# Optimization experiments

Hardware: AMD Instinct MI355X
Metric: run time of the kernel (lower is better)

Reference implementation:

```python
import jax, jax.numpy as jnp
import numpy as np

B, T_ENC, T_DEC = 64, 100, 50
L = 512      # lstm_size
E = 512      # input_encoding_size
H = 512      # att_hidden_size
R = 8        # num_review_steps
V_TOK = 30001  # token_cnt + 1 embedding rows
V_OUT = 30000  # word_cnt


def _lstm_maxout(s, c):
    # ARNet/neuraltalk2 LSTMCore: 5*L preactivations, maxout input transform
    i = jax.nn.sigmoid(s[:, :L])
    f = jax.nn.sigmoid(s[:, L:2 * L])
    o = jax.nn.sigmoid(s[:, 2 * L:3 * L])
    t = jnp.maximum(s[:, 3 * L:4 * L], s[:, 4 * L:])
    c2 = f * c + i * t
    return o * jnp.tanh(c2), c2


def _attend(feats, h, Wa2a, ba2a, Wh2a, bh2a, Watt, batt):
    # feats: [B, A, F], h: [B, L] -> context [B, F]
    p = jnp.tanh(feats @ Wa2a + ba2a + (h @ Wh2a + bh2a)[:, None, :])  # [B,A,H]
    e = jnp.squeeze(p @ Watt, -1) + batt                               # [B,A]
    a = jax.nn.softmax(e, axis=-1)
    return jnp.einsum('ba,baf->bf', a, feats)


def setup_inputs() -> dict:
    key = jax.random.key(0)
    ks = iter(jax.random.split(key, 48))
    g = lambda shape: jax.random.normal(next(ks), shape, jnp.float32) * 0.05
    z = lambda shape: jnp.zeros(shape, jnp.float32)
    return {
        'code_matrix': jax.random.randint(next(ks), (B, T_ENC), 0, V_TOK),
        'comment_matrix': jax.random.randint(next(ks), (B, T_DEC), 0, V_TOK),
        'current_comment_mask_cuda': jnp.ones((B, T_DEC), jnp.float32),
        'embed': jax.random.uniform(next(ks), (V_TOK, E), jnp.float32, -0.1, 0.1),
        'enc_Wi': g((E, 5 * L)), 'enc_bi': z((5 * L,)),
        'enc_Wh': g((L, 5 * L)), 'enc_bh': z((5 * L,)),
        'rev_Wh': g((R, L, 5 * L)), 'rev_bh': z((R, 5 * L)),
        'rev_Wa': g((R, L, 5 * L)), 'rev_ba': z((R, 5 * L)),
        'rev_Wa2a': g((R, L, H)), 'rev_ba2a': z((R, H)),
        'rev_Wh2a': g((R, L, H)), 'rev_bh2a': z((R, H)),
        'rev_Watt': g((R, H, 1)), 'rev_batt': z((R,)),
        'dec_Wi': g((E, 5 * L)), 'dec_bi': z((5 * L,)),
        'dec_Wh': g((L, 5 * L)), 'dec_bh': z((5 * L,)),
        'dec_Wa': g((L, 5 * L)), 'dec_ba': z((5 * L,)),
        'dec_Wa2a': g((L, H)), 'dec_ba2a': z((H,)),
        'dec_Wh2a': g((L, H)), 'dec_bh2a': z((H,)),
        'dec_Watt': g((H, 1)), 'dec_batt': z(()),
        'logit_W': jax.random.uniform(next(ks), (L, V_OUT), jnp.float32, -0.1, 0.1),
        'logit_b': z((V_OUT,)),
    }


def reference(code_matrix, comment_matrix, current_comment_mask_cuda, embed,
              enc_Wi, enc_bi, enc_Wh, enc_bh,
              rev_Wh, rev_bh, rev_Wa, rev_ba, rev_Wa2a, rev_ba2a,
              rev_Wh2a, rev_bh2a, rev_Watt, rev_batt,
              dec_Wi, dec_bi, dec_Wh, dec_bh, dec_Wa, dec_ba,
              dec_Wa2a, dec_ba2a, dec_Wh2a, dec_bh2a, dec_Watt, dec_batt,
              logit_W, logit_b):
    del current_comment_mask_cuda  # only used by scheduled sampling (ss_prob=0)
    Bsz = code_matrix.shape[0]
    h0 = jnp.zeros((Bsz, L), embed.dtype)
    c0 = jnp.zeros((Bsz, L), embed.dtype)

    # ---- encode ----
    enc_x = embed[code_matrix]  # [B, T_enc, E]

    def enc_step(carry, xt):
        h, c = carry
        s = xt @ enc_Wi + enc_bi + h @ enc_Wh + enc_bh
        h2, c2 = _lstm_maxout(s, c)
        return (h2, c2), h2

    (h_enc, c_enc), enc_hs = jax.lax.scan(enc_step, (h0, c0), jnp.swapaxes(enc_x, 0, 1))
    enc_hs = jnp.swapaxes(enc_hs, 0, 1)  # [B, T_enc, L]

    # ---- review (distinct params per step; scan over stacked params) ----
    def rev_step(carry, p):
        h, c = carry
        Wh, bh, Wa, ba, Wa2a, ba2a, Wh2a, bh2a, Watt, batt = p
        att_v = _attend(enc_hs, h, Wa2a, ba2a, Wh2a, bh2a, Watt, batt)
        s = h @ Wh + bh + att_v @ Wa + ba
        h2, c2 = _lstm_maxout(s, c)
        return (h2, c2), h2

    rev_params = (rev_Wh, rev_bh, rev_Wa, rev_ba, rev_Wa2a, rev_ba2a,
                  rev_Wh2a, rev_bh2a, rev_Watt, rev_batt)
    _, thought = jax.lax.scan(rev_step, (h_enc, c_enc), rev_params)
    thought = jnp.swapaxes(thought, 0, 1)  # [B, R, L]

    # ---- decode (teacher forcing; decode_state starts from encode_state) ----
    dec_x = embed[comment_matrix]  # [B, T_dec, E]

    def dec_step(carry, xt):
        h, c = carry
        att_v = _attend(thought, h, dec_Wa2a, dec_ba2a, dec_Wh2a, dec_bh2a, dec_Watt, dec_batt)
        s = xt @ dec_Wi + dec_bi + h @ dec_Wh + dec_bh + att_v @ dec_Wa + dec_ba
        h2, c2 = _lstm_maxout(s, c)
        logp = jax.nn.log_softmax(h2 @ logit_W + logit_b, axis=-1)
        return (h2, c2), logp

    _, logps = jax.lax.scan(dec_step, (h_enc, c_enc), jnp.swapaxes(dec_x, 0, 1))
    return jnp.swapaxes(logps, 0, 1)  # [B, T_dec, V_OUT]
```

## Files before the change

kernel.cpp:

```cpp
#include <hip/hip_runtime.h>
#include <math.h>
#include <stdint.h>

#define BB     64
#define TENC   100
#define TDEC   50
#define LDIM   512
#define EE     512
#define HDIM   512
#define FIVEL  2560
#define RSTEPS 8
#define VOUT   30000

typedef __attribute__((ext_vector_type(8))) short short8v;
typedef __attribute__((ext_vector_type(4))) float floatx4;

__device__ __forceinline__ float sigmoidf_(float x) { return 1.0f / (1.0f + __expf(-x)); }
__device__ __forceinline__ unsigned short f2bf(float x) {
    unsigned u = __float_as_uint(x);
    u += 0x7FFFu + ((u >> 16) & 1u);
    return (unsigned short)(u >> 16);
}
__device__ __forceinline__ float bf2f(unsigned short h) {
    return __uint_as_float(((unsigned)h) << 16);
}

__global__ __launch_bounds__(128)
void gather_embed(const float* __restrict__ embed, const int* __restrict__ tok,
                  int T, unsigned short* __restrict__ X)
{
    int m = blockIdx.x, t = m / BB, b = m % BB;
    const float* src = embed + (size_t)tok[b * T + t] * EE;
    float4 v = *(const float4*)(src + threadIdx.x * 4);
    ushort4 o = { f2bf(v.x), f2bf(v.y), f2bf(v.z), f2bf(v.w) };
    *(ushort4*)(X + (size_t)m * EE + threadIdx.x * 4) = o;
}

__global__ __launch_bounds__(256)
void conv_transpose(const float* __restrict__ W, unsigned short* __restrict__ WT,
                    int K, int N, int ldWT, int kofs)
{
    __shared__ float tile[32][33];
    int n0 = blockIdx.x * 32, k0 = blockIdx.y * 32;
    int tx = threadIdx.x & 31, ty = threadIdx.x >> 5;
    #pragma unroll
    for (int i = 0; i < 4; ++i) {
        int k = k0 + ty + i * 8, n = n0 + tx;
        tile[ty + i * 8][tx] = (n < N) ? W[(size_t)k * N + n] : 0.f;
    }
    __syncthreads();
    #pragma unroll
    for (int i = 0; i < 4; ++i) {
        int n = n0 + ty + i * 8, k = k0 + tx;
        if (n < N) WT[(size_t)n * ldWT + kofs + k] = f2bf(tile[tx][ty + i * 8]);
    }
}

__global__ __launch_bounds__(256)
void gemm_bf16(const unsigned short* __restrict__ A, const unsigned short* __restrict__ BT,
               const float* __restrict__ bias, float* __restrict__ C,
               unsigned short* __restrict__ Cb, int N, int K, long ldc, int remap)
{
    __shared__ unsigned short lds[2][128][32];
    const int tid  = threadIdx.x;
    const int wave = tid >> 6, lane = tid & 63;
    const int m0 = blockIdx.y * 128, n0 = blockIdx.x * 128;
    const int wr = wave >> 1, wc = wave & 1;

    floatx4 acc[4][4] = {};

    const int sr  = lane >> 2;
    const int scp = lane & 3;

    for (int k0 = 0; k0 < K; k0 += 32) {
        #pragma unroll
        for (int half = 0; half < 2; ++half) {
            int rbase = wave * 32 + half * 16;
            int r = rbase + sr;
            int c = scp ^ ((r >> 1) & 3);
            const unsigned short* ga = A + (size_t)(m0 + r) * K + k0 + c * 8;
            int nr = n0 + r; if (nr >= N) nr = 0;
            const unsigned short* gb = BT + (size_t)nr * K + k0 + c * 8;
            __builtin_amdgcn_global_load_lds(
                (const __attribute__((address_space(1))) void*)ga,
                (__attribute__((address_space(3))) void*)&lds[0][rbase][0], 16, 0, 0);
            __builtin_amdgcn_global_load_lds(
                (const __attribute__((address_space(1))) void*)gb,
                (__attribute__((address_space(3))) void*)&lds[1][rbase][0], 16, 0, 0);
        }
        __syncthreads();

        short8v af[4], bv[4];
        #pragma unroll
        for (int i = 0; i < 4; ++i) {
            int ra = wr * 64 + i * 16 + (lane & 15);
            int ca = (lane >> 4) ^ ((ra >> 1) & 3);
            af[i] = *(const short8v*)&lds[0][ra][ca * 8];
            int rb = wc * 64 + i * 16 + (lane & 15);
            int cb = (lane >> 4) ^ ((rb >> 1) & 3);
            bv[i] = *(const short8v*)&lds[1][rb][cb * 8];
        }
        #pragma unroll
        for (int i = 0; i < 4; ++i)
            #pragma unroll
            for (int j = 0; j < 4; ++j)
                acc[i][j] = __builtin_amdgcn_mfma_f32_16x16x32_bf16(af[i], bv[j], acc[i][j], 0, 0, 0);
        __syncthreads();
    }

    const int crow0 = m0 + wr * 64 + (lane >> 4) * 4;
    const int ccol0 = n0 + wc * 64 + (lane & 15);
    #pragma unroll
    for (int i = 0; i < 4; ++i) {
        #pragma unroll
        for (int j = 0; j < 4; ++j) {
            int col = ccol0 + j * 16;
            if (col < N) {
                float bval = bias ? bias[col] : 0.f;
                #pragma unroll
                for (int rr = 0; rr < 4; ++rr) {
                    int m = crow0 + i * 16 + rr;
                    long orow = m;
                    if (remap) { int t = m >> 6, b = m & 63; orow = (long)b * TDEC + t; }
                    float v = acc[i][j][rr] + bval;
                    if (Cb) Cb[orow * ldc + col] = f2bf(v);
                    else    C [orow * ldc + col] = v;
                }
            }
        }
    }
}

template<int NF, int MODE>
__global__ __launch_bounds__(256)
void smallgemm(const unsigned short* __restrict__ a0,
               const unsigned short* __restrict__ a1,
               const unsigned short* __restrict__ a2,
               const unsigned short* __restrict__ BT, int ldBT,
               const unsigned short* __restrict__ pre,
               const float* __restrict__ b0, const float* __restrict__ b1,
               const float* __restrict__ b2,
               const float* __restrict__ c_in, float* __restrict__ c_out,
               unsigned short* __restrict__ h_out, unsigned short* __restrict__ h_copy,
               float* __restrict__ f_out)
{
    __shared__ unsigned short Alds[64][128];
    __shared__ unsigned short Blds[NF * 16][128];
    const int tid = threadIdx.x;
    const int wave = tid >> 6, lane = tid & 63;
    const int c0 = blockIdx.x * 16;

    const unsigned short* segs[3] = {a0, a1, a2};
    const int nseg = a2 ? 3 : (a1 ? 2 : 1);
    const int NO = nseg * 4;

    floatx4 acc[NF];
    #pragma unroll
    for (int g = 0; g < NF; ++g) acc[g] = (floatx4){0.f, 0.f, 0.f, 0.f};

    short8v ra[4], rb[NF];

    #define LOAD_TILE(ot_) do {                                                \
        int seg_ = (ot_) >> 2, k0_ = ((ot_) & 3) * 128;                        \
        const unsigned short* A_ = segs[seg_];                                 \
        _Pragma("unroll")                                                      \
        for (int j = 0; j < 4; ++j) {                                          \
            int idx = tid + j * 256; int r = idx >> 4, ch = idx & 15;          \
            ra[j] = *(const short8v*)(A_ + (size_t)r * 512 + k0_ + ch * 8);    \
        }                                                                      \
        _Pragma("unroll")                                                      \
        for (int j = 0; j < NF; ++j) {                                         \
            int idx = tid + j * 256; int r = idx >> 4, ch = idx & 15;          \
            int grow = (r >> 4) * 512 + c0 + (r & 15);                         \
            rb[j] = *(const short8v*)(BT + (size_t)grow * ldBT + seg_ * 512 + k0_ + ch * 8); \
        }                                                                      \
    } while (0)

    LOAD_TILE(0);
    for (int ot = 0; ot < NO; ++ot) {
        __syncthreads();
        #pragma unroll
        for (int j = 0; j < 4; ++j) {
            int idx = tid + j * 256; int r = idx >> 4, ch = idx & 15;
            *(short8v*)&Alds[r][(ch ^ (r & 7)) * 8] = ra[j];
        }
        #pragma unroll
        for (int j = 0; j < NF; ++j) {
            int idx = tid + j * 256; int r = idx >> 4, ch = idx & 15;
            *(short8v*)&Blds[r][(ch ^ (r & 7)) * 8] = rb[j];
        }
        __syncthreads();
        if (ot + 1 < NO) LOAD_TILE(ot + 1);

        const int arow = wave * 16 + (lane & 15);
        const int q = lane >> 4;
        #pragma unroll
        for (int kk = 0; kk < 4; ++kk) {
            int ch = kk * 4 + q;
            short8v af = *(const short8v*)&Alds[arow][(ch ^ (arow & 7)) * 8];
            #pragma unroll
            for (int g = 0; g < NF; ++g) {
                int brow = g * 16 + (lane & 15);
                short8v bf = *(const short8v*)&Blds[brow][(ch ^ (brow & 7)) * 8];
                acc[g] = __builtin_amdgcn_mfma_f32_16x16x32_bf16(af, bf, acc[g], 0, 0, 0);
            }
        }
    }
    #undef LOAD_TILE

    const int m = wave * 16 + (lane >> 4) * 4;
    const int c = c0 + (lane & 15);
    if (MODE == 1) {
        float bv = b0 ? b0[c] : 0.f;
        #pragma unroll
        for (int rr = 0; rr < 4; ++rr)
            f_out[(size_t)(m + rr) * 512 + c] = acc[0][rr] + bv;
    } else {
        float bias[5];
        #pragma unroll
        for (int g = 0; g < 5; ++g) {
            float v = b0[g * 512 + c];
            if (b1) v += b1[g * 512 + c];
            if (b2) v += b2[g * 512 + c];
            bias[g] = v;
        }
        #pragma unroll
        for (int rr = 0; rr < 4; ++rr) {
            int row = m + rr;
            float s[5];
            #pragma unroll
            for (int g = 0; g < 5; ++g) {
                s[g] = acc[g][rr] + bias[g];
                if (pre) s[g] += bf2f(pre[(size_t)row * FIVEL + g * 512 + c]);
            }
            float ig = sigmoidf_(s[0]), fg = sigmoidf_(s[1]), og = sigmoidf_(s[2]);
            float tt = fmaxf(s[3], s[4]);
            float c2 = fg * c_in[(size_t)row * 512 + c] + ig * tt;
            float h2 = og * tanhf(c2);
            c_out[(size_t)row * 512 + c] = c2;
            unsigned short hb = f2bf(h2);
            h_out[(size_t)row * 512 + c] = hb;
            if (h_copy) h_copy[(size_t)row * 512 + c] = hb;
        }
    }
}

__global__ __launch_bounds__(256)
void attend(const unsigned short* __restrict__ proj, const float* __restrict__ hproj,
            const unsigned short* __restrict__ feats, const float* __restrict__ Watt,
            unsigned short* __restrict__ att_v, int A)
{
    __shared__ float hp[512];
    __shared__ float wa[512];
    __shared__ float ealpha[128];
    const int b = blockIdx.x;
    const int tid = threadIdx.x;
    for (int i = tid; i < 512; i += 256) { hp[i] = hproj[b * HDIM + i]; wa[i] = Watt[i]; }
    __syncthreads();
    const int wave = tid >> 6, lane = tid & 63;
    for (int a = wave; a < A; a += 4) {
        short8v pv = *(const short8v*)(proj + ((size_t)a * BB + b) * HDIM + lane * 8);
        float e = 0.f;
        #pragma unroll
        for (int j = 0; j < 8; ++j) {
            int hcol = lane * 8 + j;
            e += tanhf(bf2f((unsigned short)pv[j]) + hp[hcol]) * wa[hcol];
        }
        #pragma unroll
        for (int off = 32; off; off >>= 1) e += __shfl_xor(e, off);
        if (lane == 0) ealpha[a] = e;
    }
    __syncthreads();
    if (wave == 0) {
        float v1 = (lane < A) ? ealpha[lane] : -3.0e38f;
        float v2 = (lane + 64 < A) ? ealpha[lane + 64] : -3.0e38f;
        float m = fmaxf(v1, v2);
        #pragma unroll
        for (int off = 32; off; off >>= 1) m = fmaxf(m, __shfl_xor(m, off));
        float x1 = (lane < A) ? __expf(v1 - m) : 0.f;
        float x2 = (lane + 64 < A) ? __expf(v2 - m) : 0.f;
        float ssum = x1 + x2;
        #pragma unroll
        for (int off = 32; off; off >>= 1) ssum += __shfl_xor(ssum, off);
        float inv = 1.0f / ssum;
        if (lane < A) ealpha[lane] = x1 * inv;
        if (lane + 64 < A) ealpha[lane + 64] = x2 * inv;
    }
    __syncthreads();
    #pragma unroll
    for (int jj = 0; jj < 2; ++jj) {
        int l = tid + jj * 256;
        float acc = 0.f;
        for (int a = 0; a < A; ++a)
            acc += ealpha[a] * bf2f(feats[((size_t)a * BB + b) * LDIM + l]);
        att_v[(size_t)b * LDIM + l] = f2bf(acc);
    }
}

__global__ __launch_bounds__(256)
void log_softmax_(float* __restrict__ out)
{
    float* row = out + (size_t)blockIdx.x * VOUT;
    const int tid = threadIdx.x;
    float m = -3.0e38f, s = 0.f;
    for (int i = tid; i < VOUT / 4; i += 256) {
        float4 x = ((const float4*)row)[i];
        float xs[4] = {x.x, x.y, x.z, x.w};
        #pragma unroll
        for (int q = 0; q < 4; ++q) {
            float v = xs[q];
            if (v > m) { s = s * __expf(m - v) + 1.0f; m = v; }
            else       { s += __expf(v - m); }
        }
    }
    #pragma unroll
    for (int off = 32; off; off >>= 1) {
        float mo = __shfl_xor(m, off);
        float so = __shfl_xor(s, off);
        float mn = fmaxf(m, mo);
        s = s * __expf(m - mn) + so * __expf(mo - mn);
        m = mn;
    }
    __shared__ float ms[4], ss[4];
    const int wave = tid >> 6, lane = tid & 63;
    if (lane == 0) { ms[wave] = m; ss[wave] = s; }
    __syncthreads();
    float M2 = fmaxf(fmaxf(ms[0], ms[1]), fmaxf(ms[2], ms[3]));
    float S2 = ss[0] * __expf(ms[0] - M2) + ss[1] * __expf(ms[1] - M2) +
               ss[2] * __expf(ms[2] - M2) + ss[3] * __expf(ms[3] - M2);
    float lse = M2 + __logf(S2);
    for (int i = tid; i < VOUT / 4; i += 256) {
        float4 x = ((const float4*)row)[i];
        x.x -= lse; x.y -= lse; x.z -= lse; x.w -= lse;
        ((float4*)row)[i] = x;
    }
}

extern "C" void kernel_launch(void* const* d_in, const int* in_sizes, int n_in,
                              void* d_out_, int out_size, void* d_ws, size_t ws_size,
                              hipStream_t stream)
{
    const int*   code     = (const int*)  d_in[0];
    const int*   comment  = (const int*)  d_in[1];
    const float* embed    = (const float*)d_in[3];
    const float* enc_Wi   = (const float*)d_in[4];
    const float* enc_bi   = (const float*)d_in[5];
    const float* enc_Wh   = (const float*)d_in[6];
    const float* enc_bh   = (const float*)d_in[7];
    const float* rev_Wh   = (const float*)d_in[8];
    const float* rev_bh   = (const float*)d_in[9];
    const float* rev_Wa   = (const float*)d_in[10];
    const float* rev_ba   = (const float*)d_in[11];
    const float* rev_Wa2a = (const float*)d_in[12];
    const float* rev_ba2a = (const float*)d_in[13];
    const float* rev_Wh2a = (const float*)d_in[14];
    const float* rev_bh2a = (const float*)d_in[15];
    const float* rev_Watt = (const float*)d_in[16];
    const float* dec_Wi   = (const float*)d_in[18];
    const float* dec_bi   = (const float*)d_in[19];
    const float* dec_Wh   = (const float*)d_in[20];
    const float* dec_bh   = (const float*)d_in[21];
    const float* dec_Wa   = (const float*)d_in[22];
    const float* dec_ba   = (const float*)d_in[23];
    const float* dec_Wa2a = (const float*)d_in[24];
    const float* dec_ba2a = (const float*)d_in[25];
    const float* dec_Wh2a = (const float*)d_in[26];
    const float* dec_bh2a = (const float*)d_in[27];
    const float* dec_Watt = (const float*)d_in[28];
    const float* logit_W  = (const float*)d_in[30];
    const float* logit_b  = (const float*)d_in[31];
    float* out = (float*)d_out_;

    float* ws = (float*)d_ws;
    size_t off = 0;

    float* X = ws; off += 8192000;
    unsigned short* enc_pre_b = (unsigned short*)X;
    unsigned short* logit_WT  = (unsigned short*)X;

    float* U = ws + off; off += 2293760;
    unsigned short* WiT_enc    = (unsigned short*)U;
    unsigned short* enc_x_b    = (unsigned short*)(U + 655360);
    unsigned short* rev_proj_b = (unsigned short*)U;
    unsigned short* dec_h_b    = (unsigned short*)U;

    unsigned short* enc_hs_b = (unsigned short*)(ws + off); off += 1638400;
    unsigned short* encWhT   = (unsigned short*)(ws + off); off += 655360;
    unsigned short* revWcomb = (unsigned short*)(ws + off); off += 10485760;
    unsigned short* decWcomb = (unsigned short*)(ws + off); off += 1966080;
    unsigned short* revWT    = (unsigned short*)(ws + off); off += 1048576;
    unsigned short* decWT    = (unsigned short*)(ws + off); off += 131072;
    unsigned short* revWh2aT = (unsigned short*)(ws + off); off += 1048576;
    unsigned short* decWh2aT = (unsigned short*)(ws + off); off += 131072;
    unsigned short* dec_x_b  = (unsigned short*)(ws + off); off += 819200;
    unsigned short* thought_b= (unsigned short*)(ws + off); off += 131072;
    unsigned short* tproj_b  = (unsigned short*)(ws + off); off += 131072;
    unsigned short* h0_b     = (unsigned short*)(ws + off); off += 16384;
    unsigned short* hb0      = (unsigned short*)(ws + off); off += 16384;
    unsigned short* hb1      = (unsigned short*)(ws + off); off += 16384;
    unsigned short* attv_b   = (unsigned short*)(ws + off); off += 16384;
    float* cbuf[4];
    for (int i = 0; i < 4; ++i) { cbuf[i] = ws + off; off += 32768; }
    float* hproj = ws + off; off += 32768;
    if (ws_size < off * sizeof(float)) return;

    unsigned short* hb[2] = {hb0, hb1};
    const dim3 blk(256);

    hipMemsetAsync(cbuf[0], 0, (size_t)BB * LDIM * sizeof(float), stream);
    hipMemsetAsync(h0_b, 0, (size_t)BB * LDIM * sizeof(unsigned short), stream);

    gather_embed<<<TENC * BB, 128, 0, stream>>>(embed, code, TENC, enc_x_b);
    gather_embed<<<TDEC * BB, 128, 0, stream>>>(embed, comment, TDEC, dec_x_b);
    conv_transpose<<<dim3(80, 16), blk, 0, stream>>>(enc_Wi, WiT_enc, 512, FIVEL, 512, 0);
    conv_transpose<<<dim3(80, 16), blk, 0, stream>>>(enc_Wh, encWhT, 512, FIVEL, 512, 0);
    for (int r = 0; r < RSTEPS; ++r) {
        conv_transpose<<<dim3(80, 16), blk, 0, stream>>>(
            rev_Wh + (size_t)r * 1310720, revWcomb + (size_t)r * 2621440, 512, FIVEL, 1024, 0);
        conv_transpose<<<dim3(80, 16), blk, 0, stream>>>(
            rev_Wa + (size_t)r * 1310720, revWcomb + (size_t)r * 2621440, 512, FIVEL, 1024, 512);
        conv_transpose<<<dim3(16, 16), blk, 0, stream>>>(
            rev_Wa2a + (size_t)r * 262144, revWT + (size_t)r * 262144, 512, 512, 512, 0);
        conv_transpose<<<dim3(16, 16), blk, 0, stream>>>(
            rev_Wh2a + (size_t)r * 262144, revWh2aT + (size_t)r * 262144, 512, 512, 512, 0);
    }
    conv_transpose<<<dim3(80, 16), blk, 0, stream>>>(dec_Wi, decWcomb, 512, FIVEL, 1536, 0);
    conv_transpose<<<dim3(80, 16), blk, 0, stream>>>(dec_Wh, decWcomb, 512, FIVEL, 1536, 512);
    conv_transpose<<<dim3(80, 16), blk, 0, stream>>>(dec_Wa, decWcomb, 512, FIVEL, 1536, 1024);
    conv_transpose<<<dim3(16, 16), blk, 0, stream>>>(dec_Wa2a, decWT, 512, 512, 512, 0);
    conv_transpose<<<dim3(16, 16), blk, 0, stream>>>(dec_Wh2a, decWh2aT, 512, 512, 512, 0);

    gemm_bf16<<<dim3(FIVEL / 128, TENC * BB / 128), blk, 0, stream>>>(
        enc_x_b, WiT_enc, enc_bi, nullptr, enc_pre_b, FIVEL, EE, FIVEL, 0);

    for (int t = 0; t < TENC; ++t) {
        const unsigned short* hin = (t == 0) ? h0_b : enc_hs_b + (size_t)(t - 1) * 32768;
        smallgemm<5, 0><<<32, blk, 0, stream>>>(
            hin, nullptr, nullptr, encWhT, 512,
            enc_pre_b + (size_t)t * BB * FIVEL,
            enc_bh, nullptr, nullptr,
            cbuf[t & 1], cbuf[(t + 1) & 1],
            enc_hs_b + (size_t)t * 32768, nullptr, nullptr);
    }
    const unsigned short* h_enc = enc_hs_b + (size_t)(TENC - 1) * 32768;

    conv_transpose<<<dim3((VOUT + 31) / 32, 16), blk, 0, stream>>>(
        logit_W, logit_WT, 512, VOUT, 512, 0);

    const unsigned short* rh = h_enc;
    for (int r = 0; r < RSTEPS; ++r) {
        gemm_bf16<<<dim3(4, 50), blk, 0, stream>>>(
            enc_hs_b, revWT + (size_t)r * 262144, rev_ba2a + (size_t)r * HDIM,
            nullptr, rev_proj_b, HDIM, LDIM, HDIM, 0);
        smallgemm<1, 1><<<32, blk, 0, stream>>>(
            rh, nullptr, nullptr, revWh2aT + (size_t)r * 262144, 512,
            nullptr, rev_bh2a + (size_t)r * HDIM, nullptr, nullptr,
            nullptr, nullptr, nullptr, nullptr, hproj);
        attend<<<BB, blk, 0, stream>>>(rev_proj_b, hproj, enc_hs_b,
                                       rev_Watt + (size_t)r * HDIM, attv_b, TENC);
        const float* ci = (r == 0) ? cbuf[0] : cbuf[2 + ((r - 1) & 1)];
        smallgemm<5, 0><<<32, blk, 0, stream>>>(
            rh, attv_b, nullptr, revWcomb + (size_t)r * 2621440, 1024,
            nullptr, rev_bh + (size_t)r * FIVEL, rev_ba + (size_t)r * FIVEL, nullptr,
            ci, cbuf[2 + (r & 1)],
            hb[r & 1], thought_b + (size_t)r * 32768, nullptr);
        rh = hb[r & 1];
    }

    gemm_bf16<<<dim3(4, 4), blk, 0, stream>>>(
        thought_b, decWT, dec_ba2a, nullptr, tproj_b, HDIM, LDIM, HDIM, 0);

    const unsigned short* dh = h_enc;
    for (int t = 0; t < TDEC; ++t) {
        smallgemm<1, 1><<<32, blk, 0, stream>>>(
            dh, nullptr, nullptr, decWh2aT, 512,
            nullptr, dec_bh2a, nullptr, nullptr,
            nullptr, nullptr, nullptr, nullptr, hproj);
        attend<<<BB, blk, 0, stream>>>(tproj_b, hproj, thought_b, dec_Watt, attv_b, RSTEPS);
        const float* ci = (t == 0) ? cbuf[0] : cbuf[2 + ((t - 1) & 1)];
        smallgemm<5, 0><<<32, blk, 0, stream>>>(
            dec_x_b + (size_t)t * 32768, dh, attv_b, decWcomb, 1536,
            nullptr, dec_bi, dec_bh, dec_ba,
            ci, cbuf[2 + (t & 1)],
            hb[t & 1], dec_h_b + (size_t)t * 32768, nullptr);
        dh = hb[t & 1];
    }

    gemm_bf16<<<dim3((VOUT + 127) / 128, TDEC * BB / 128), blk, 0, stream>>>(
        dec_h_b, logit_WT, logit_b, out, nullptr, VOUT, LDIM, VOUT, 1);
    log_softmax_<<<TDEC * BB, blk, 0, stream>>>(out);
}
```

Before: 4.012 ms.

## Fuse recurrent LSTM loops into persistent kernels with grid barriers

Replaces the per-timestep launches of the encoder, review and decoder recurrences with three persistent kernels that sync between steps through a global atomic barrier. Cell state stays in registers, and attention plus the h2a projection are fused per pair of batch rows. The change also batches the review-step projection GEMM across all steps, merges the weight transposes into z-batched launches, and uses a fast exp-based tanh. The aim is to remove hundreds of kernel launch gaps; the cost is reliance on all blocks being co-resident for the spin barrier, and workspace buffers are now aliased.

```diff
diff --git a/kernel.cpp b/kernel.cpp
--- a/kernel.cpp
+++ b/kernel.cpp
@@ -14,8 +14,33 @@
 
 typedef __attribute__((ext_vector_type(8))) short short8v;
 typedef __attribute__((ext_vector_type(4))) float floatx4;
+typedef unsigned short ushort_t;
+
+static const size_t OFF_A        = 0;
+static const size_t OFF_WIT_ENC  = 8192000;
+static const size_t OFF_ENCX     = 8847360;
+static const size_t OFF_LOGWT    = 0;
+static const size_t OFF_DECH     = 7680000;
+static const size_t OFF_ENC_HS   = 13107200;
+static const size_t OFF_ENC_WHT  = 14745600;
+static const size_t OFF_REVWC    = 15400960;
+static const size_t OFF_DECWC    = 25886720;
+static const size_t OFF_REVWT    = 27852800;
+static const size_t OFF_DECWT    = 28901376;
+static const size_t OFF_REVWH2AT = 29032448;
+static const size_t OFF_DECWH2AT = 30081024;
+static const size_t OFF_DECX     = 30212096;
+static const size_t OFF_THOUGHT  = 31031296;
+static const size_t OFF_TPROJ    = 31162368;
+static const size_t OFF_HB0      = 31293440;
+static const size_t OFF_HB1      = 31309824;
+static const size_t OFF_ATTV     = 31326208;
+static const size_t OFF_CENC     = 31342592;
+static const size_t OFF_BAR      = 31375360;
+static const size_t WS_TOTAL     = 31375376;
 
 __device__ __forceinline__ float sigmoidf_(float x) { return 1.0f / (1.0f + __expf(-x)); }
+__device__ __forceinline__ float tanh_fast(float x) { return 1.0f - 2.0f / (__expf(2.0f * x) + 1.0f); }
 __device__ __forceinline__ unsigned short f2bf(float x) {
     unsigned u = __float_as_uint(x);
     u += 0x7FFFu + ((u >> 16) & 1u);
@@ -25,9 +50,28 @@
     return __uint_as_float(((unsigned)h) << 16);
 }
 
+__device__ __forceinline__ void gbar(unsigned int* bar, int nblk)
+{
+    __threadfence();
+    __syncthreads();
+    if (threadIdx.x == 0) {
+        unsigned int g = __hip_atomic_load(&bar[1], __ATOMIC_RELAXED, __HIP_MEMORY_SCOPE_AGENT);
+        unsigned int v = __hip_atomic_fetch_add(&bar[0], 1u, __ATOMIC_ACQ_REL, __HIP_MEMORY_SCOPE_AGENT);
+        if (v == (unsigned int)(nblk - 1)) {
+            __hip_atomic_store(&bar[0], 0u, __ATOMIC_RELAXED, __HIP_MEMORY_SCOPE_AGENT);
+            __hip_atomic_fetch_add(&bar[1], 1u, __ATOMIC_RELEASE, __HIP_MEMORY_SCOPE_AGENT);
+        } else {
+            while (__hip_atomic_load(&bar[1], __ATOMIC_RELAXED, __HIP_MEMORY_SCOPE_AGENT) == g)
+                __builtin_amdgcn_s_sleep(2);
+        }
+    }
+    __syncthreads();
+    __threadfence();
+}
+
 __global__ __launch_bounds__(128)
 void gather_embed(const float* __restrict__ embed, const int* __restrict__ tok,
-                  int T, unsigned short* __restrict__ X)
+                  int T, ushort_t* __restrict__ X)
 {
     int m = blockIdx.x, t = m / BB, b = m % BB;
     const float* src = embed + (size_t)tok[b * T + t] * EE;
@@ -37,9 +81,11 @@
 }
 
 __global__ __launch_bounds__(256)
-void conv_transpose(const float* __restrict__ W, unsigned short* __restrict__ WT,
-                    int K, int N, int ldWT, int kofs)
-{
+void conv_transpose(const float* __restrict__ W, ushort_t* __restrict__ WT,
+                    int N, int ldWT, int kofs, long Wz, long WTz)
+{
+    W  += (size_t)blockIdx.z * Wz;
+    WT += (size_t)blockIdx.z * WTz;
     __shared__ float tile[32][33];
     int n0 = blockIdx.x * 32, k0 = blockIdx.y * 32;
     int tx = threadIdx.x & 31, ty = threadIdx.x >> 5;
@@ -57,18 +103,17 @@
 }
 
 __global__ __launch_bounds__(256)
-void gemm_bf16(const unsigned short* __restrict__ A, const unsigned short* __restrict__ BT,
+void gemm_bf16(const ushort_t* __restrict__ A, const ushort_t* __restrict__ BT,
                const float* __restrict__ bias, float* __restrict__ C,
-               unsigned short* __restrict__ Cb, int N, int K, long ldc, int remap)
-{
-    __shared__ unsigned short lds[2][128][32];
+               ushort_t* __restrict__ Cb, int N, int K, long ldc, int remap)
+{
+    __shared__ ushort_t lds[2][128][32];
     const int tid  = threadIdx.x;
     const int wave = tid >> 6, lane = tid & 63;
     const int m0 = blockIdx.y * 128, n0 = blockIdx.x * 128;
     const int wr = wave >> 1, wc = wave & 1;
 
     floatx4 acc[4][4] = {};
-
     const int sr  = lane >> 2;
     const int scp = lane & 3;
 
@@ -78,9 +123,9 @@
             int rbase = wave * 32 + half * 16;
             int r = rbase + sr;
             int c = scp ^ ((r >> 1) & 3);
-            const unsigned short* ga = A + (size_t)(m0 + r) * K + k0 + c * 8;
+            const ushort_t* ga = A + (size_t)(m0 + r) * K + k0 + c * 8;
             int nr = n0 + r; if (nr >= N) nr = 0;
-            const unsigned short* gb = BT + (size_t)nr * K + k0 + c * 8;
+            const ushort_t* gb = BT + (size_t)nr * K + k0 + c * 8;
             __builtin_amdgcn_global_load_lds(
                 (const __attribute__((address_space(1))) void*)ga,
                 (__attribute__((address_space(3))) void*)&lds[0][rbase][0], 16, 0, 0);
@@ -131,67 +176,49 @@
     }
 }
 
-template<int NF, int MODE>
-__global__ __launch_bounds__(256)
-void smallgemm(const unsigned short* __restrict__ a0,
-               const unsigned short* __restrict__ a1,
-               const unsigned short* __restrict__ a2,
-               const unsigned short* __restrict__ BT, int ldBT,
-               const unsigned short* __restrict__ pre,
-               const float* __restrict__ b0, const float* __restrict__ b1,
-               const float* __restrict__ b2,
-               const float* __restrict__ c_in, float* __restrict__ c_out,
-               unsigned short* __restrict__ h_out, unsigned short* __restrict__ h_copy,
-               float* __restrict__ f_out)
-{
-    __shared__ unsigned short Alds[64][128];
-    __shared__ unsigned short Blds[NF * 16][128];
+__device__ __forceinline__ void lstm_accum(
+    const ushort_t* __restrict__ Aseg,
+    const ushort_t* __restrict__ BT,
+    const int ldBT, const int segk, const int c0, floatx4* acc,
+    ushort_t (*Alds)[128], ushort_t (*Blds)[128])
+{
     const int tid = threadIdx.x;
     const int wave = tid >> 6, lane = tid & 63;
-    const int c0 = blockIdx.x * 16;
-
-    const unsigned short* segs[3] = {a0, a1, a2};
-    const int nseg = a2 ? 3 : (a1 ? 2 : 1);
-    const int NO = nseg * 4;
-
-    floatx4 acc[NF];
-    #pragma unroll
-    for (int g = 0; g < NF; ++g) acc[g] = (floatx4){0.f, 0.f, 0.f, 0.f};
-
-    short8v ra[4], rb[NF];
-
-    #define LOAD_TILE(ot_) do {                                                \
-        int seg_ = (ot_) >> 2, k0_ = ((ot_) & 3) * 128;                        \
-        const unsigned short* A_ = segs[seg_];                                 \
-        _Pragma("unroll")                                                      \
-        for (int j = 0; j < 4; ++j) {                                          \
-            int idx = tid + j * 256; int r = idx >> 4, ch = idx & 15;          \
-            ra[j] = *(const short8v*)(A_ + (size_t)r * 512 + k0_ + ch * 8);    \
-        }                                                                      \
-        _Pragma("unroll")                                                      \
-        for (int j = 0; j < NF; ++j) {                                         \
-            int idx = tid + j * 256; int r = idx >> 4, ch = idx & 15;          \
-            int grow = (r >> 4) * 512 + c0 + (r & 15);                         \
-            rb[j] = *(const short8v*)(BT + (size_t)grow * ldBT + seg_ * 512 + k0_ + ch * 8); \
-        }                                                                      \
-    } while (0)
-
-    LOAD_TILE(0);
-    for (int ot = 0; ot < NO; ++ot) {
+    short8v ra[4], rb[5];
+    const ushort_t* ap[4]; ushort_t* aw[4];
+    const ushort_t* bp[5]; ushort_t* bw[5];
+    #pragma unroll
+    for (int j = 0; j < 4; ++j) {
+        int idx = tid + j * 256, r = idx >> 4, ch = idx & 15;
+        ap[j] = Aseg + (size_t)r * 512 + ch * 8;
+        aw[j] = &Alds[r][(ch ^ (r & 7)) * 8];
+    }
+    #pragma unroll
+    for (int j = 0; j < 5; ++j) {
+        int idx = tid + j * 256, r = idx >> 4, ch = idx & 15;
+        int grow = (r >> 4) * 512 + c0 + (r & 15);
+        bp[j] = BT + (size_t)grow * ldBT + segk + ch * 8;
+        bw[j] = &Blds[r][(ch ^ (r & 7)) * 8];
+    }
+    #pragma unroll
+    for (int j = 0; j < 4; ++j) ra[j] = *(const short8v*)ap[j];
+    #pragma unroll
+    for (int j = 0; j < 5; ++j) rb[j] = *(const short8v*)bp[j];
+
+    #pragma unroll 1
+    for (int ot = 0; ot < 4; ++ot) {
         __syncthreads();
         #pragma unroll
-        for (int j = 0; j < 4; ++j) {
-            int idx = tid + j * 256; int r = idx >> 4, ch = idx & 15;
-            *(short8v*)&Alds[r][(ch ^ (r & 7)) * 8] = ra[j];
-        }
-        #pragma unroll
-        for (int j = 0; j < NF; ++j) {
-            int idx = tid + j * 256; int r = idx >> 4, ch = idx & 15;
-            *(short8v*)&Blds[r][(ch ^ (r & 7)) * 8] = rb[j];
-        }
+        for (int j = 0; j < 4; ++j) *(short8v*)aw[j] = ra[j];
+        #pragma unroll
+        for (int j = 0; j < 5; ++j) *(short8v*)bw[j] = rb[j];
         __syncthreads();
-        if (ot + 1 < NO) LOAD_TILE(ot + 1);
-
+        if (ot < 3) {
+            #pragma unroll
+            for (int j = 0; j < 4; ++j) ra[j] = *(const short8v*)(ap[j] + (ot + 1) * 128);
+            #pragma unroll
+            for (int j = 0; j < 5; ++j) rb[j] = *(const short8v*)(bp[j] + (ot + 1) * 128);
+        }
         const int arow = wave * 16 + (lane & 15);
         const int q = lane >> 4;
         #pragma unroll
@@ -199,101 +226,272 @@
             int ch = kk * 4 + q;
             short8v af = *(const short8v*)&Alds[arow][(ch ^ (arow & 7)) * 8];
             #pragma unroll
-            for (int g = 0; g < NF; ++g) {
+            for (int g = 0; g < 5; ++g) {
                 int brow = g * 16 + (lane & 15);
                 short8v bf = *(const short8v*)&Blds[brow][(ch ^ (brow & 7)) * 8];
                 acc[g] = __builtin_amdgcn_mfma_f32_16x16x32_bf16(af, bf, acc[g], 0, 0, 0);
             }
         }
     }
-    #undef LOAD_TILE
-
+}
+
+__device__ __forceinline__ void lstm_epilogue(
+    floatx4* acc, const float* b0, const float* b1, const float* b2,
+    const ushort_t* pre, float* creg, float* c_store,
+    ushort_t* h_out, ushort_t* h_copy, int c0)
+{
+    const int tid = threadIdx.x, wave = tid >> 6, lane = tid & 63;
     const int m = wave * 16 + (lane >> 4) * 4;
     const int c = c0 + (lane & 15);
-    if (MODE == 1) {
-        float bv = b0 ? b0[c] : 0.f;
-        #pragma unroll
-        for (int rr = 0; rr < 4; ++rr)
-            f_out[(size_t)(m + rr) * 512 + c] = acc[0][rr] + bv;
-    } else {
-        float bias[5];
+    float bias[5];
+    #pragma unroll
+    for (int g = 0; g < 5; ++g) {
+        float v = b0[g * 512 + c];
+        if (b1) v += b1[g * 512 + c];
+        if (b2) v += b2[g * 512 + c];
+        bias[g] = v;
+    }
+    #pragma unroll
+    for (int rr = 0; rr < 4; ++rr) {
+        int row = m + rr;
+        float s[5];
         #pragma unroll
         for (int g = 0; g < 5; ++g) {
-            float v = b0[g * 512 + c];
-            if (b1) v += b1[g * 512 + c];
-            if (b2) v += b2[g * 512 + c];
-            bias[g] = v;
-        }
-        #pragma unroll
-        for (int rr = 0; rr < 4; ++rr) {
-            int row = m + rr;
-            float s[5];
+            s[g] = acc[g][rr] + bias[g];
+            if (pre) s[g] += bf2f(pre[(size_t)row * FIVEL + g * 512 + c]);
+        }
+        float ig = sigmoidf_(s[0]), fg = sigmoidf_(s[1]), og = sigmoidf_(s[2]);
+        float tt = fmaxf(s[3], s[4]);
+        float c2 = fg * creg[rr] + ig * tt;
+        float h2 = og * tanh_fast(c2);
+        creg[rr] = c2;
+        ushort_t hb_ = f2bf(h2);
+        h_out[(size_t)row * 512 + c] = hb_;
+        if (h_copy) h_copy[(size_t)row * 512 + c] = hb_;
+        if (c_store) c_store[(size_t)row * 512 + c] = c2;
+    }
+}
+
+struct AttSm {
+    ushort_t hl[2][512];
+    float hp[2][512];
+    float wa[512];
+    float ealpha[2][128];
+};
+
+__device__ void attend_fused(const ushort_t* __restrict__ hprev,
+    const ushort_t* __restrict__ projBase, long projLd,
+    const ushort_t* __restrict__ feats,
+    const ushort_t* __restrict__ W2aT, const float* __restrict__ b2a,
+    const float* __restrict__ Watt, ushort_t* __restrict__ attv,
+    int A, int b0, char* smraw)
+{
+    AttSm* sm = (AttSm*)smraw;
+    const int tid = threadIdx.x;
+    {
+        int i4 = tid * 4;
+        int bi = i4 >> 9, k = i4 & 511;
+        *(ushort4*)&sm->hl[bi][k] = *(const ushort4*)(hprev + (size_t)(b0 + bi) * 512 + k);
+        sm->wa[tid] = Watt[tid];
+        sm->wa[tid + 256] = Watt[tid + 256];
+    }
+    __syncthreads();
+    #pragma unroll
+    for (int half = 0; half < 2; ++half) {
+        int n = tid + half * 256;
+        float a0 = b2a[n], a1 = a0;
+        const ushort_t* wrow = W2aT + (size_t)n * 512;
+        #pragma unroll 4
+        for (int k8 = 0; k8 < 64; ++k8) {
+            short8v w  = *(const short8v*)(wrow + k8 * 8);
+            short8v h0 = *(const short8v*)&sm->hl[0][k8 * 8];
+            short8v h1 = *(const short8v*)&sm->hl[1][k8 * 8];
             #pragma unroll
-            for (int g = 0; g < 5; ++g) {
-                s[g] = acc[g][rr] + bias[g];
-                if (pre) s[g] += bf2f(pre[(size_t)row * FIVEL + g * 512 + c]);
+            for (int e = 0; e < 8; ++e) {
+                float wf = bf2f((ushort_t)w[e]);
+                a0 += wf * bf2f((ushort_t)h0[e]);
+                a1 += wf * bf2f((ushort_t)h1[e]);
             }
-            float ig = sigmoidf_(s[0]), fg = sigmoidf_(s[1]), og = sigmoidf_(s[2]);
-            float tt = fmaxf(s[3], s[4]);
-            float c2 = fg * c_in[(size_t)row * 512 + c] + ig * tt;
-            float h2 = og * tanhf(c2);
-            c_out[(size_t)row * 512 + c] = c2;
-            unsigned short hb = f2bf(h2);
-            h_out[(size_t)row * 512 + c] = hb;
-            if (h_copy) h_copy[(size_t)row * 512 + c] = hb;
-        }
-    }
-}
-
-__global__ __launch_bounds__(256)
-void attend(const unsigned short* __restrict__ proj, const float* __restrict__ hproj,
-            const unsigned short* __restrict__ feats, const float* __restrict__ Watt,
-            unsigned short* __restrict__ att_v, int A)
-{
-    __shared__ float hp[512];
-    __shared__ float wa[512];
-    __shared__ float ealpha[128];
-    const int b = blockIdx.x;
-    const int tid = threadIdx.x;
-    for (int i = tid; i < 512; i += 256) { hp[i] = hproj[b * HDIM + i]; wa[i] = Watt[i]; }
+        }
+        sm->hp[0][n] = a0;
+        sm->hp[1][n] = a1;
+    }
     __syncthreads();
     const int wave = tid >> 6, lane = tid & 63;
-    for (int a = wave; a < A; a += 4) {
-        short8v pv = *(const short8v*)(proj + ((size_t)a * BB + b) * HDIM + lane * 8);
+    for (int idx = wave; idx < 2 * A; idx += 4) {
+        int a = idx >> 1, bi = idx & 1;
+        short8v pv = *(const short8v*)(projBase + ((size_t)a * 64 + b0 + bi) * projLd + lane * 8);
         float e = 0.f;
         #pragma unroll
         for (int j = 0; j < 8; ++j) {
-            int hcol = lane * 8 + j;
-            e += tanhf(bf2f((unsigned short)pv[j]) + hp[hcol]) * wa[hcol];
+            int h = lane * 8 + j;
+            e += tanh_fast(bf2f((ushort_t)pv[j]) + sm->hp[bi][h]) * sm->wa[h];
         }
         #pragma unroll
         for (int off = 32; off; off >>= 1) e += __shfl_xor(e, off);
-        if (lane == 0) ealpha[a] = e;
-    }
-    __syncthreads();
-    if (wave == 0) {
-        float v1 = (lane < A) ? ealpha[lane] : -3.0e38f;
-        float v2 = (lane + 64 < A) ? ealpha[lane + 64] : -3.0e38f;
-        float m = fmaxf(v1, v2);
-        #pragma unroll
-        for (int off = 32; off; off >>= 1) m = fmaxf(m, __shfl_xor(m, off));
-        float x1 = (lane < A) ? __expf(v1 - m) : 0.f;
-        float x2 = (lane + 64 < A) ? __expf(v2 - m) : 0.f;
-        float ssum = x1 + x2;
-        #pragma unroll
-        for (int off = 32; off; off >>= 1) ssum += __shfl_xor(ssum, off);
-        float inv = 1.0f / ssum;
-        if (lane < A) ealpha[lane] = x1 * inv;
-        if (lane + 64 < A) ealpha[lane + 64] = x2 * inv;
-    }
-    __syncthreads();
-    #pragma unroll
-    for (int jj = 0; jj < 2; ++jj) {
-        int l = tid + jj * 256;
-        float acc = 0.f;
-        for (int a = 0; a < A; ++a)
-            acc += ealpha[a] * bf2f(feats[((size_t)a * BB + b) * LDIM + l]);
-        att_v[(size_t)b * LDIM + l] = f2bf(acc);
+        if (lane == 0) sm->ealpha[bi][a] = e;
+    }
+    __syncthreads();
+    if (wave < 2) {
+        int bi = wave;
+        float v1 = (lane < A) ? sm->ealpha[bi][lane] : -3.0e38f;
+        float v2 = (lane + 64 < A) ? sm->ealpha[bi][lane + 64] : -3.0e38f;
+        float mm = fmaxf(v1, v2);
+        #pragma unroll
+        for (int off = 32; off; off >>= 1) mm = fmaxf(mm, __shfl_xor(mm, off));
+        float x1 = (lane < A) ? __expf(v1 - mm) : 0.f;
+        float x2 = (lane + 64 < A) ? __expf(v2 - mm) : 0.f;
+        float ss = x1 + x2;
+        #pragma unroll
+        for (int off = 32; off; off >>= 1) ss += __shfl_xor(ss, off);
+        float inv = 1.f / ss;
+        if (lane < A) sm->ealpha[bi][lane] = x1 * inv;
+        if (lane + 64 < A) sm->ealpha[bi][lane + 64] = x2 * inv;
+    }
+    __syncthreads();
+    #pragma unroll
+    for (int bi = 0; bi < 2; ++bi) {
+        int b = b0 + bi;
+        float s0 = 0.f, s1 = 0.f;
+        for (int a = 0; a < A; ++a) {
+            float al = sm->ealpha[bi][a];
+            unsigned int u = *(const unsigned int*)(feats + ((size_t)a * 64 + b) * 512 + tid * 2);
+            s0 += al * bf2f((ushort_t)(u & 0xffffu));
+            s1 += al * bf2f((ushort_t)(u >> 16));
+        }
+        ushort2 o = { f2bf(s0), f2bf(s1) };
+        *(ushort2*)(attv + (size_t)b * 512 + tid * 2) = o;
+    }
+}
+
+__global__ __launch_bounds__(256, 1)
+void enc_scan(float* ws, const float* __restrict__ enc_bh)
+{
+    __shared__ __align__(16) char smraw[36864];
+    ushort_t (*Alds)[128] = (ushort_t(*)[128])smraw;
+    ushort_t (*Blds)[128] = (ushort_t(*)[128])(smraw + 16384);
+    const ushort_t* encWhT  = (const ushort_t*)(ws + OFF_ENC_WHT);
+    const ushort_t* enc_pre = (const ushort_t*)(ws + OFF_A);
+    ushort_t* enc_hs = (ushort_t*)(ws + OFF_ENC_HS);
+    float* cenc = ws + OFF_CENC;
+    unsigned int* bar = (unsigned int*)(ws + OFF_BAR);
+    const int c0 = blockIdx.x * 16;
+    float creg[4] = {0.f, 0.f, 0.f, 0.f};
+
+    #pragma unroll 1
+    for (int t = 0; t < TENC; ++t) {
+        floatx4 acc[5] = {};
+        if (t > 0)
+            lstm_accum(enc_hs + (size_t)(t - 1) * 32768, encWhT, 512, 0, c0, acc, Alds, Blds);
+        lstm_epilogue(acc, enc_bh, nullptr, nullptr,
+                      enc_pre + (size_t)t * 163840, creg,
+                      (t == TENC - 1) ? cenc : nullptr,
+                      enc_hs + (size_t)t * 32768, nullptr, c0);
+        gbar(bar, gridDim.x);
+    }
+}
+
+__global__ __launch_bounds__(256, 1)
+void rev_scan(float* ws, const float* __restrict__ rev_bh, const float* __restrict__ rev_ba,
+              const float* __restrict__ rev_bh2a, const float* __restrict__ rev_Watt)
+{
+    __shared__ __align__(16) char smraw[36864];
+    ushort_t (*Alds)[128] = (ushort_t(*)[128])smraw;
+    ushort_t (*Blds)[128] = (ushort_t(*)[128])(smraw + 16384);
+    const ushort_t* revWc = (const ushort_t*)(ws + OFF_REVWC);
+    const ushort_t* revWh2aT = (const ushort_t*)(ws + OFF_REVWH2AT);
+    const ushort_t* rev_proj = (const ushort_t*)(ws + OFF_A);
+    const ushort_t* enc_hs = (const ushort_t*)(ws + OFF_ENC_HS);
+    ushort_t* thought = (ushort_t*)(ws + OFF_THOUGHT);
+    ushort_t* attv = (ushort_t*)(ws + OFF_ATTV);
+    ushort_t* hb[2] = { (ushort_t*)(ws + OFF_HB0), (ushort_t*)(ws + OFF_HB1) };
+    const float* cenc = ws + OFF_CENC;
+    unsigned int* bar = (unsigned int*)(ws + OFF_BAR);
+    const int blk = blockIdx.x;
+    const int c0 = (blk & 31) * 16;
+    const ushort_t* h_enc = enc_hs + (size_t)(TENC - 1) * 32768;
+
+    float creg[4] = {0.f, 0.f, 0.f, 0.f};
+    if (blk < 32) {
+        const int tid = threadIdx.x, wave = tid >> 6, lane = tid & 63;
+        const int m = wave * 16 + (lane >> 4) * 4, c = c0 + (lane & 15);
+        #pragma unroll
+        for (int rr = 0; rr < 4; ++rr) creg[rr] = cenc[(size_t)(m + rr) * 512 + c];
+    }
+
+    const ushort_t* rh = h_enc;
+    #pragma unroll 1
+    for (int r = 0; r < RSTEPS; ++r) {
+        floatx4 acc[5] = {};
+        if (blk < 32) {
+            lstm_accum(rh, revWc + (size_t)r * 2621440, 1024, 0, c0, acc, Alds, Blds);
+        } else {
+            attend_fused(rh, rev_proj + (size_t)r * 512, 4096, enc_hs,
+                         revWh2aT + (size_t)r * 262144, rev_bh2a + r * 512,
+                         rev_Watt + r * 512, attv, TENC, (blk - 32) * 2, smraw);
+        }
+        gbar(bar, gridDim.x);
+        if (blk < 32) {
+            lstm_accum(attv, revWc + (size_t)r * 2621440, 1024, 512, c0, acc, Alds, Blds);
+            lstm_epilogue(acc, rev_bh + (size_t)r * FIVEL, rev_ba + (size_t)r * FIVEL, nullptr,
+                          nullptr, creg, nullptr, hb[r & 1],
+                          thought + (size_t)r * 32768, c0);
+        }
+        gbar(bar, gridDim.x);
+        rh = hb[r & 1];
+    }
+}
+
+__global__ __launch_bounds__(256, 1)
+void dec_scan(float* ws, const float* __restrict__ dec_bi, const float* __restrict__ dec_bh,
+              const float* __restrict__ dec_ba, const float* __restrict__ dec_bh2a,
+              const float* __restrict__ dec_Watt)
+{
+    __shared__ __align__(16) char smraw[36864];
+    ushort_t (*Alds)[128] = (ushort_t(*)[128])smraw;
+    ushort_t (*Blds)[128] = (ushort_t(*)[128])(smraw + 16384);
+    const ushort_t* decWc = (const ushort_t*)(ws + OFF_DECWC);
+    const ushort_t* decWh2aT = (const ushort_t*)(ws + OFF_DECWH2AT);
+    const ushort_t* tproj = (const ushort_t*)(ws + OFF_TPROJ);
+    const ushort_t* thought = (const ushort_t*)(ws + OFF_THOUGHT);
+    const ushort_t* dec_x = (const ushort_t*)(ws + OFF_DECX);
+    const ushort_t* enc_hs = (const ushort_t*)(ws + OFF_ENC_HS);
+    ushort_t* dec_h = (ushort_t*)(ws + OFF_DECH);
+    ushort_t* attv = (ushort_t*)(ws + OFF_ATTV);
+    ushort_t* hb[2] = { (ushort_t*)(ws + OFF_HB0), (ushort_t*)(ws + OFF_HB1) };
+    const float* cenc = ws + OFF_CENC;
+    unsigned int* bar = (unsigned int*)(ws + OFF_BAR);
+    const int blk = blockIdx.x;
+    const int c0 = (blk & 31) * 16;
+    const ushort_t* h_enc = enc_hs + (size_t)(TENC - 1) * 32768;
+
+    float creg[4] = {0.f, 0.f, 0.f, 0.f};
+    if (blk < 32) {
+        const int tid = threadIdx.x, wave = tid >> 6, lane = tid & 63;
+        const int m = wave * 16 + (lane >> 4) * 4, c = c0 + (lane & 15);
+        #pragma unroll
+        for (int rr = 0; rr < 4; ++rr) creg[rr] = cenc[(size_t)(m + rr) * 512 + c];
+    }
+
+    const ushort_t* dh = h_enc;
+    #pragma unroll 1
+    for (int t = 0; t < TDEC; ++t) {
+        floatx4 acc[5] = {};
+        if (blk < 32) {
+            lstm_accum(dec_x + (size_t)t * 32768, decWc, 1536, 0, c0, acc, Alds, Blds);
+            lstm_accum(dh, decWc, 1536, 512, c0, acc, Alds, Blds);
+        } else {
+            attend_fused(dh, tproj, 512, thought, decWh2aT, dec_bh2a,
+                         dec_Watt, attv, RSTEPS, (blk - 32) * 2, smraw);
+        }
+        gbar(bar, gridDim.x);
+        if (blk < 32) {
+            lstm_accum(attv, decWc, 1536, 1024, c0, acc, Alds, Blds);
+            lstm_epilogue(acc, dec_bi, dec_bh, dec_ba, nullptr, creg, nullptr,
+                          hb[t & 1], dec_h + (size_t)t * 32768, c0);
+        }
+        gbar(bar, gridDim.x);
+        dh = hb[t & 1];
     }
 }
 
@@ -372,119 +570,60 @@
     float* out = (float*)d_out_;
 
     float* ws = (float*)d_ws;
-    size_t off = 0;
-
-    float* X = ws; off += 8192000;
-    unsigned short* enc_pre_b = (unsigned short*)X;
-    unsigned short* logit_WT  = (unsigned short*)X;
-
-    float* U = ws + off; off += 2293760;
-    unsigned short* WiT_enc    = (unsigned short*)U;
-    unsigned short* enc_x_b    = (unsigned short*)(U + 655360);
-    unsigned short* rev_proj_b = (unsigned short*)U;
-    unsigned short* dec_h_b    = (unsigned short*)U;
-
-    unsigned short* enc_hs_b = (unsigned short*)(ws + off); off += 1638400;
-    unsigned short* encWhT   = (unsigned short*)(ws + off); off += 655360;
-    unsigned short* revWcomb = (unsigned short*)(ws + off); off += 10485760;
-    unsigned short* decWcomb = (unsigned short*)(ws + off); off += 1966080;
-    unsigned short* revWT    = (unsigned short*)(ws + off); off += 1048576;
-    unsigned short* decWT    = (unsigned short*)(ws + off); off += 131072;
-    unsigned short* revWh2aT = (unsigned short*)(ws + off); off += 1048576;
-    unsigned short* decWh2aT = (unsigned short*)(ws + off); off += 131072;
-    unsigned short* dec_x_b  = (unsigned short*)(ws + off); off += 819200;
-    unsigned short* thought_b= (unsigned short*)(ws + off); off += 131072;
-    unsigned short* tproj_b  = (unsigned short*)(ws + off); off += 131072;
-    unsigned short* h0_b     = (unsigned short*)(ws + off); off += 16384;
-    unsigned short* hb0      = (unsigned short*)(ws + off); off += 16384;
-    unsigned short* hb1      = (unsigned short*)(ws + off); off += 16384;
-    unsigned short* attv_b   = (unsigned short*)(ws + off); off += 16384;
-    float* cbuf[4];
-    for (int i = 0; i < 4; ++i) { cbuf[i] = ws + off; off += 32768; }
-    float* hproj = ws + off; off += 32768;
-    if (ws_size < off * sizeof(float)) return;
-
-    unsigned short* hb[2] = {hb0, hb1};
+    if (ws_size < WS_TOTAL * sizeof(float)) return;
+
+    ushort_t* enc_pre_b   = (ushort_t*)(ws + OFF_A);
+    ushort_t* rev_projA   = (ushort_t*)(ws + OFF_A);
+    ushort_t* logit_WT    = (ushort_t*)(ws + OFF_LOGWT);
+    ushort_t* dec_h_b     = (ushort_t*)(ws + OFF_DECH);
+    ushort_t* WiT_enc     = (ushort_t*)(ws + OFF_WIT_ENC);
+    ushort_t* enc_x_b     = (ushort_t*)(ws + OFF_ENCX);
+    ushort_t* enc_hs_b    = (ushort_t*)(ws + OFF_ENC_HS);
+    ushort_t* encWhT      = (ushort_t*)(ws + OFF_ENC_WHT);
+    ushort_t* revWcomb    = (ushort_t*)(ws + OFF_REVWC);
+    ushort_t* decWcomb    = (ushort_t*)(ws + OFF_DECWC);
+    ushort_t* revWT       = (ushort_t*)(ws + OFF_REVWT);
+    ushort_t* decWT       = (ushort_t*)(ws + OFF_DECWT);
+    ushort_t* revWh2aT    = (ushort_t*)(ws + OFF_REVWH2AT);
+    ushort_t* decWh2aT    = (ushort_t*)(ws + OFF_DECWH2AT);
+    ushort_t* dec_x_b     = (ushort_t*)(ws + OFF_DECX);
+    ushort_t* thought_b   = (ushort_t*)(ws + OFF_THOUGHT);
+    ushort_t* tproj_b     = (ushort_t*)(ws + OFF_TPROJ);
+
     const dim3 blk(256);
 
-    hipMemsetAsync(cbuf[0], 0, (size_t)BB * LDIM * sizeof(float), stream);
-    hipMemsetAsync(h0_b, 0, (size_t)BB * LDIM * sizeof(unsigned short), stream);
+    hipMemsetAsync((char*)d_ws + OFF_BAR * sizeof(float), 0, 8, stream);
 
     gather_embed<<<TENC * BB, 128, 0, stream>>>(embed, code, TENC, enc_x_b);
     gather_embed<<<TDEC * BB, 128, 0, stream>>>(embed, comment, TDEC, dec_x_b);
-    conv_transpose<<<dim3(80, 16), blk, 0, stream>>>(enc_Wi, WiT_enc, 512, FIVEL, 512, 0);
-    conv_transpose<<<dim3(80, 16), blk, 0, stream>>>(enc_Wh, encWhT, 512, FIVEL, 512, 0);
-    for (int r = 0; r < RSTEPS; ++r) {
-        conv_transpose<<<dim3(80, 16), blk, 0, stream>>>(
-            rev_Wh + (size_t)r * 1310720, revWcomb + (size_t)r * 2621440, 512, FIVEL, 1024, 0);
-        conv_transpose<<<dim3(80, 16), blk, 0, stream>>>(
-            rev_Wa + (size_t)r * 1310720, revWcomb + (size_t)r * 2621440, 512, FIVEL, 1024, 512);
-        conv_transpose<<<dim3(16, 16), blk, 0, stream>>>(
-            rev_Wa2a + (size_t)r * 262144, revWT + (size_t)r * 262144, 512, 512, 512, 0);
-        conv_transpose<<<dim3(16, 16), blk, 0, stream>>>(
-            rev_Wh2a + (size_t)r * 262144, revWh2aT + (size_t)r * 262144, 512, 512, 512, 0);
-    }
-    conv_transpose<<<dim3(80, 16), blk, 0, stream>>>(dec_Wi, decWcomb, 512, FIVEL, 1536, 0);
-    conv_transpose<<<dim3(80, 16), blk, 0, stream>>>(dec_Wh, decWcomb, 512, FIVEL, 1536, 512);
-    conv_transpose<<<dim3(80, 16), blk, 0, stream>>>(dec_Wa, decWcomb, 512, FIVEL, 1536, 1024);
-    conv_transpose<<<dim3(16, 16), blk, 0, stream>>>(dec_Wa2a, decWT, 512, 512, 512, 0);
-    conv_transpose<<<dim3(16, 16), blk, 0, stream>>>(dec_Wh2a, decWh2aT, 512, 512, 512, 0);
+    conv_transpose<<<dim3(80, 16, 1), blk, 0, stream>>>(enc_Wi, WiT_enc, FIVEL, 512, 0, 0, 0);
+    conv_transpose<<<dim3(80, 16, 1), blk, 0, stream>>>(enc_Wh, encWhT, FIVEL, 512, 0, 0, 0);
+    conv_transpose<<<dim3(80, 16, 8), blk, 0, stream>>>(rev_Wh, revWcomb, FIVEL, 1024, 0,    1310720, 2621440);
+    conv_transpose<<<dim3(80, 16, 8), blk, 0, stream>>>(rev_Wa, revWcomb, FIVEL, 1024, 512,  1310720, 2621440);
+    conv_transpose<<<dim3(16, 16, 8), blk, 0, stream>>>(rev_Wa2a, revWT, 512, 512, 0,        262144, 262144);
+    conv_transpose<<<dim3(16, 16, 8), blk, 0, stream>>>(rev_Wh2a, revWh2aT, 512, 512, 0,     262144, 262144);
+    conv_transpose<<<dim3(80, 16, 1), blk, 0, stream>>>(dec_Wi, decWcomb, FIVEL, 1536, 0, 0, 0);
+    conv_transpose<<<dim3(80, 16, 1), blk, 0, stream>>>(dec_Wh, decWcomb, FIVEL, 1536, 512, 0, 0);
+    conv_transpose<<<dim3(80, 16, 1), blk, 0, stream>>>(dec_Wa, decWcomb, FIVEL, 1536, 1024, 0, 0);
+    conv_transpose<<<dim3(16, 16, 1), blk, 0, stream>>>(dec_Wa2a, decWT, 512, 512, 0, 0, 0);
+    conv_transpose<<<dim3(16, 16, 1), blk, 0, stream>>>(dec_Wh2a, decWh2aT, 512, 512, 0, 0, 0);
 
     gemm_bf16<<<dim3(FIVEL / 128, TENC * BB / 128), blk, 0, stream>>>(
         enc_x_b, WiT_enc, enc_bi, nullptr, enc_pre_b, FIVEL, EE, FIVEL, 0);
 
-    for (int t = 0; t < TENC; ++t) {
-        const unsigned short* hin = (t == 0) ? h0_b : enc_hs_b + (size_t)(t - 1) * 32768;
-        smallgemm<5, 0><<<32, blk, 0, stream>>>(
-            hin, nullptr, nullptr, encWhT, 512,
-            enc_pre_b + (size_t)t * BB * FIVEL,
-            enc_bh, nullptr, nullptr,
-            cbuf[t & 1], cbuf[(t + 1) & 1],
-            enc_hs_b + (size_t)t * 32768, nullptr, nullptr);
-    }
-    const unsigned short* h_enc = enc_hs_b + (size_t)(TENC - 1) * 32768;
-
-    conv_transpose<<<dim3((VOUT + 31) / 32, 16), blk, 0, stream>>>(
-        logit_W, logit_WT, 512, VOUT, 512, 0);
-
-    const unsigned short* rh = h_enc;
-    for (int r = 0; r < RSTEPS; ++r) {
-        gemm_bf16<<<dim3(4, 50), blk, 0, stream>>>(
-            enc_hs_b, revWT + (size_t)r * 262144, rev_ba2a + (size_t)r * HDIM,
-            nullptr, rev_proj_b, HDIM, LDIM, HDIM, 0);
-        smallgemm<1, 1><<<32, blk, 0, stream>>>(
-            rh, nullptr, nullptr, revWh2aT + (size_t)r * 262144, 512,
-            nullptr, rev_bh2a + (size_t)r * HDIM, nullptr, nullptr,
-            nullptr, nullptr, nullptr, nullptr, hproj);
-        attend<<<BB, blk, 0, stream>>>(rev_proj_b, hproj, enc_hs_b,
-                                       rev_Watt + (size_t)r * HDIM, attv_b, TENC);
-        const float* ci = (r == 0) ? cbuf[0] : cbuf[2 + ((r - 1) & 1)];
-        smallgemm<5, 0><<<32, blk, 0, stream>>>(
-            rh, attv_b, nullptr, revWcomb + (size_t)r * 2621440, 1024,
-            nullptr, rev_bh + (size_t)r * FIVEL, rev_ba + (size_t)r * FIVEL, nullptr,
-            ci, cbuf[2 + (r & 1)],
-            hb[r & 1], thought_b + (size_t)r * 32768, nullptr);
-        rh = hb[r & 1];
-    }
+    enc_scan<<<32, blk, 0, stream>>>(ws, enc_bh);
+
+    gemm_bf16<<<dim3(32, 50), blk, 0, stream>>>(
+        enc_hs_b, revWT, rev_ba2a, nullptr, rev_projA, 4096, LDIM, 4096, 0);
+
+    rev_scan<<<64, blk, 0, stream>>>(ws, rev_bh, rev_ba, rev_bh2a, rev_Watt);
 
     gemm_bf16<<<dim3(4, 4), blk, 0, stream>>>(
         thought_b, decWT, dec_ba2a, nullptr, tproj_b, HDIM, LDIM, HDIM, 0);
-
-    const unsigned short* dh = h_enc;
-    for (int t = 0; t < TDEC; ++t) {
-        smallgemm<1, 1><<<32, blk, 0, stream>>>(
-            dh, nullptr, nullptr, decWh2aT, 512,
-            nullptr, dec_bh2a, nullptr, nullptr,
-            nullptr, nullptr, nullptr, nullptr, hproj);
-        attend<<<BB, blk, 0, stream>>>(tproj_b, hproj, thought_b, dec_Watt, attv_b, RSTEPS);
-        const float* ci = (t == 0) ? cbuf[0] : cbuf[2 + ((t - 1) & 1)];
-        smallgemm<5, 0><<<32, blk, 0, stream>>>(
-            dec_x_b + (size_t)t * 32768, dh, attv_b, decWcomb, 1536,
-            nullptr, dec_bi, dec_bh, dec_ba,
-            ci, cbuf[2 + (t & 1)],
-            hb[t & 1], dec_h_b + (size_t)t * 32768, nullptr);
-        dh = hb[t & 1];
-    }
+    conv_transpose<<<dim3((VOUT + 31) / 32, 16, 1), blk, 0, stream>>>(
+        logit_W, logit_WT, VOUT, 512, 0, 0, 0);
+
+    dec_scan<<<64, blk, 0, stream>>>(ws, dec_bi, dec_bh, dec_ba, dec_bh2a, dec_Watt);
 
     gemm_bf16<<<dim3((VOUT + 127) / 128, TDEC * BB / 128), blk, 0, stream>>>(
         dec_h_b, logit_WT, logit_b, out, nullptr, VOUT, LDIM, VOUT, 1);
```

Measured after the change: 5.899 ms. 47.0% more time.
